# Kernel optimization log

Hardware: AMD Instinct MI355X
Metric: run time of the kernel (lower is better)

## Reference

```python
import jax, jax.numpy as jnp
import numpy as np

MARGIN = 0.2  # self.margin; temperature is unused in the original forward


def setup_inputs() -> dict:
    key = jax.random.key(0)
    k1, k2 = jax.random.split(key)
    B, D, NUM_CLASSES = 512, 256, 10
    features = jax.random.normal(k1, (B, D), dtype=jnp.float32)
    labels = jax.random.randint(k2, (B,), 0, NUM_CLASSES, dtype=jnp.int32)
    return {"features": features, "labels": labels}


def reference(features, labels):
    B = features.shape[0]
    sim = features @ features.T  # [B, B]

    eq = (labels[:, None] == labels[None, :])
    pos_mask = eq.astype(sim.dtype) * (1.0 - jnp.eye(B, dtype=sim.dtype))  # diag zeroed
    neg_mask = 1.0 - eq.astype(sim.dtype)

    # For anchor row i, pos j, neg k: relu(margin + sim[i,k] - sim[i,j])
    hinge = jax.nn.relu(MARGIN + sim[:, None, :] - sim[:, :, None])  # [B, Bpos, Bneg]
    loss_sum = jnp.einsum('ijk,ij,ik->', hinge, pos_mask, neg_mask)

    pos_cnt = pos_mask.sum(axis=1)  # per-row positive counts
    neg_cnt = neg_mask.sum(axis=1)
    valid = (pos_cnt > 0) & (neg_cnt > 0)
    num_valid = valid.sum().astype(sim.dtype)

    # Original bug faithfully reproduced: denominator uses the LAST row's
    # pos/neg counts (pos_sim/neg_sim leak out of the python loop).
    denom = num_valid * pos_cnt[-1] * neg_cnt[-1]
    return jnp.where(denom > 0, loss_sum / denom, jnp.zeros((), sim.dtype))
```

## Files before the change

kernel.cpp:

```cpp
#include <hip/hip_runtime.h>

#define B 512
#define D 256
#define NCLS 10
#define MARGIN 0.2f
#define THREADS 1024
#define NWAVES (THREADS / 64)
#define ROWS 2
#define NBLOCKS (B / ROWS)
#define DT 32
#define NDT (D / DT)
#define TILE_FLOATS (B * DT)

__global__ __launch_bounds__(THREADS) void fused_loss_kernel(
    const float* __restrict__ F, const int* __restrict__ labels,
    float* __restrict__ out)
{
    __shared__ float  buf[2][TILE_FLOATS];
    __shared__ float  fi[ROWS][D];
    __shared__ float  pos_vals[ROWS][B + 4];
    __shared__ float  neg_vals[ROWS][B];
    __shared__ int    lbl[B];
    __shared__ int    cnt[ROWS][2];
    __shared__ int    hist[NCLS];
    __shared__ float  wred[NWAVES];
    __shared__ int    vred[NWAVES];

    const int t    = threadIdx.x;
    const int lane = t & 63;
    const int w    = t >> 6;
    const int i0   = blockIdx.x * ROWS;
    const int q    = t & 3;
    const int g    = t >> 2;
    const int j0   = 2 * g;
    const int j1   = 2 * g + 1;
    const int s0   = (j0 & 7) ^ ((j0 >> 3) & 7);
    const int s1   = (j1 & 7) ^ ((j1 >> 3) & 7);

    auto stage = [&](float* dstbase, int tile) {
#pragma unroll
        for (int k = 0; k < 4; ++k) {
            const int p  = (w << 8) + (k << 6) + lane;
            const int jj = p >> 3;
            const int e4 = (p & 7) ^ (jj & 7) ^ ((jj >> 3) & 7);
            const float* src = F + jj * D + tile * DT + (e4 << 2);
            float* dst = dstbase + (w << 10) + (k << 8);
            __builtin_amdgcn_global_load_lds(
                (const __attribute__((address_space(1))) void*)src,
                (__attribute__((address_space(3))) void*)dst, 16, 0, 0);
        }
    };

    if (t < B)        lbl[t] = labels[t];
    if (t < NCLS)     hist[t] = 0;
    if (t < ROWS * 2) ((int*)cnt)[t] = 0;
    if (t < (ROWS * D) / 4)
        ((float4*)fi)[t] = ((const float4*)(F + (size_t)i0 * D))[t];
    stage(buf[0], 0);

    asm volatile("s_waitcnt lgkmcnt(0)" ::: "memory");
    __builtin_amdgcn_s_barrier();

    if (t < B) atomicAdd(&hist[lbl[t]], 1);

    float acc00 = 0.f, acc01 = 0.f, acc10 = 0.f, acc11 = 0.f;
    int cur = 0;
    for (int tile = 0; tile < NDT; ++tile) {
        if (tile + 1 < NDT) {
            stage(buf[cur ^ 1], tile + 1);
            asm volatile("s_waitcnt vmcnt(4)" ::: "memory");
        } else {
            asm volatile("s_waitcnt vmcnt(0)" ::: "memory");
        }
        __builtin_amdgcn_s_barrier();
        __builtin_amdgcn_sched_barrier(0);
        const float* bufc = buf[cur];
        const int dt = tile * DT;
#pragma unroll
        for (int k = 0; k < 2; ++k) {
            const int e4 = 2 * q + k;
            const float4 x0 = *(const float4*)&bufc[(j0 << 5) + ((e4 ^ s0) << 2)];
            const float4 x1 = *(const float4*)&bufc[(j1 << 5) + ((e4 ^ s1) << 2)];
            const float4 a0 = *(const float4*)&fi[0][dt + (e4 << 2)];
            const float4 a1 = *(const float4*)&fi[1][dt + (e4 << 2)];
            acc00 = fmaf(a0.x, x0.x, acc00); acc00 = fmaf(a0.y, x0.y, acc00);
            acc00 = fmaf(a0.z, x0.z, acc00); acc00 = fmaf(a0.w, x0.w, acc00);
            acc01 = fmaf(a1.x, x0.x, acc01); acc01 = fmaf(a1.y, x0.y, acc01);
            acc01 = fmaf(a1.z, x0.z, acc01); acc01 = fmaf(a1.w, x0.w, acc01);
            acc10 = fmaf(a0.x, x1.x, acc10); acc10 = fmaf(a0.y, x1.y, acc10);
            acc10 = fmaf(a0.z, x1.z, acc10); acc10 = fmaf(a0.w, x1.w, acc10);
            acc11 = fmaf(a1.x, x1.x, acc11); acc11 = fmaf(a1.y, x1.y, acc11);
            acc11 = fmaf(a1.z, x1.z, acc11); acc11 = fmaf(a1.w, x1.w, acc11);
        }
        __builtin_amdgcn_sched_barrier(0);
        __builtin_amdgcn_s_barrier();
        cur ^= 1;
    }

    float2* part = (float2*)buf[0];
    part[(q << 9) + j0] = make_float2(acc00, acc01);
    part[(q << 9) + j1] = make_float2(acc10, acc11);
    __syncthreads();
    const int j = t & (B - 1);
    const int h = t >> 9;
    const float2 p0 = part[(0 << 9) + j];
    const float2 p1 = part[(1 << 9) + j];
    const float2 p2 = part[(2 << 9) + j];
    const float2 p3 = part[(3 << 9) + j];
    const float sv = h ? (p0.y + p1.y + p2.y + p3.y)
                       : (p0.x + p1.x + p2.x + p3.x);

    {
        bool valid = false;
        if (t < B) { const int c = hist[lbl[t]]; valid = (c >= 2) && (c <= B - 1); }
        const unsigned long long mv = __ballot(valid);
        if (lane == 0) vred[w] = __popcll(mv);
    }

    const int r   = h;
    const int i_r = i0 + r;
    const int li  = lbl[i_r];
    {
        const bool active = (j != i_r);
        const bool ispos  = active && (lbl[j] == li);
        const bool isneg  = active && (lbl[j] != li);
        const unsigned long long mp = __ballot(ispos);
        const unsigned long long mn = __ballot(isneg);
        int basep = 0, basen = 0;
        if (lane == 0) {
            basep = atomicAdd(&cnt[r][0], __popcll(mp));
            basen = atomicAdd(&cnt[r][1], __popcll(mn));
        }
        basep = __shfl(basep, 0, 64);
        basen = __shfl(basen, 0, 64);
        const unsigned long long below = (1ull << lane) - 1ull;
        if (ispos) pos_vals[r][basep + __popcll(mp & below)] = sv;
        if (isneg) neg_vals[r][basen + __popcll(mn & below)] = sv;
    }
    __syncthreads();
    const int P = cnt[r][0], N = cnt[r][1];
    if (j < 4) pos_vals[r][P + j] = 1e30f;
    __syncthreads();

    const float nv_t = (j < N) ? neg_vals[r][j] : -1e30f;
    float local = 0.f;
    for (int pi = 0; pi < P; pi += 4) {
        const float4 pv = *(const float4*)&pos_vals[r][pi];
        float v;
        v = nv_t - (pv.x - MARGIN); local += (v > 0.f) ? v : 0.f;
        v = nv_t - (pv.y - MARGIN); local += (v > 0.f) ? v : 0.f;
        v = nv_t - (pv.z - MARGIN); local += (v > 0.f) ? v : 0.f;
        v = nv_t - (pv.w - MARGIN); local += (v > 0.f) ? v : 0.f;
    }

#pragma unroll
    for (int off = 32; off > 0; off >>= 1)
        local += __shfl_down(local, off, 64);
    if (lane == 0) wred[w] = local;
    __syncthreads();
    if (t == 0) {
        float s = 0.f;
        int   nv = 0;
#pragma unroll
        for (int k = 0; k < NWAVES; ++k) { s += wred[k]; nv += vred[k]; }
        const int   clast = hist[lbl[B - 1]];
        const float denom = (float)nv * (float)(clast - 1) * (float)(B - clast);
        atomicAdd(out, (denom > 0.f) ? s / denom : 0.f);
    }
}

extern "C" void kernel_launch(void* const* d_in, const int* in_sizes, int n_in,
                              void* d_out, int out_size, void* d_ws, size_t ws_size,
                              hipStream_t stream) {
    const float* F      = (const float*)d_in[0];
    const int*   labels = (const int*)d_in[1];
    float* out = (float*)d_out;
    (void)d_ws; (void)ws_size;

    fused_loss_kernel<<<NBLOCKS, THREADS, 0, stream>>>(F, labels, out);
}
```

Before: 67.87 us.

## Load anchor rows via scalar loads and remap threads to wave-uniform k-slices

Removes the LDS copy of the two anchor feature rows. Each wave now reads its anchor-row slice directly into scalar registers with s_load_dwordx4, which relies on the thread-to-work mapping being redone so the quarter of the k dimension (rq) is uniform across a wave. Per-tile LDS traffic drops to just the column tiles, and the anchor values come from SGPRs at the cost of scalar-cache loads every tile and an explicit lgkmcnt wait. The change also shifts the column-tile bank-access pattern, which could affect conflicts.

```diff
diff --git a/kernel.cpp b/kernel.cpp
--- a/kernel.cpp
+++ b/kernel.cpp
@@ -12,12 +12,13 @@
 #define NDT (D / DT)
 #define TILE_FLOATS (B * DT)
 
+typedef float f32x4 __attribute__((ext_vector_type(4)));
+
 __global__ __launch_bounds__(THREADS) void fused_loss_kernel(
     const float* __restrict__ F, const int* __restrict__ labels,
     float* __restrict__ out)
 {
     __shared__ float  buf[2][TILE_FLOATS];
-    __shared__ float  fi[ROWS][D];
     __shared__ float  pos_vals[ROWS][B + 4];
     __shared__ float  neg_vals[ROWS][B];
     __shared__ int    lbl[B];
@@ -30,8 +31,8 @@
     const int lane = t & 63;
     const int w    = t >> 6;
     const int i0   = blockIdx.x * ROWS;
-    const int q    = t & 3;
-    const int g    = t >> 2;
+    const int rq   = __builtin_amdgcn_readfirstlane(w & 3);
+    const int g    = ((w >> 2) << 6) + lane;
     const int j0   = 2 * g;
     const int j1   = 2 * g + 1;
     const int s0   = (j0 & 7) ^ ((j0 >> 3) & 7);
@@ -54,14 +55,15 @@
     if (t < B)        lbl[t] = labels[t];
     if (t < NCLS)     hist[t] = 0;
     if (t < ROWS * 2) ((int*)cnt)[t] = 0;
-    if (t < (ROWS * D) / 4)
-        ((float4*)fi)[t] = ((const float4*)(F + (size_t)i0 * D))[t];
     stage(buf[0], 0);
 
     asm volatile("s_waitcnt lgkmcnt(0)" ::: "memory");
     __builtin_amdgcn_s_barrier();
 
     if (t < B) atomicAdd(&hist[lbl[t]], 1);
+
+    const uint64_t sbase =
+        (uint64_t)(const void*)(F + (size_t)i0 * D + 8 * rq);
 
     float acc00 = 0.f, acc01 = 0.f, acc10 = 0.f, acc11 = 0.f;
     int cur = 0;
@@ -74,32 +76,51 @@
         }
         __builtin_amdgcn_s_barrier();
         __builtin_amdgcn_sched_barrier(0);
+
+        const uint64_t sb = sbase + (uint64_t)(tile * DT * 4);
+        f32x4 a00, a01, a10, a11;
+        asm volatile("s_load_dwordx4 %0, %1, 0x0"   : "=s"(a00) : "s"(sb));
+        asm volatile("s_load_dwordx4 %0, %1, 0x10"  : "=s"(a01) : "s"(sb));
+        asm volatile("s_load_dwordx4 %0, %1, 0x400" : "=s"(a10) : "s"(sb));
+        asm volatile("s_load_dwordx4 %0, %1, 0x410" : "=s"(a11) : "s"(sb));
+
         const float* bufc = buf[cur];
-        const int dt = tile * DT;
-#pragma unroll
-        for (int k = 0; k < 2; ++k) {
-            const int e4 = 2 * q + k;
-            const float4 x0 = *(const float4*)&bufc[(j0 << 5) + ((e4 ^ s0) << 2)];
-            const float4 x1 = *(const float4*)&bufc[(j1 << 5) + ((e4 ^ s1) << 2)];
-            const float4 a0 = *(const float4*)&fi[0][dt + (e4 << 2)];
-            const float4 a1 = *(const float4*)&fi[1][dt + (e4 << 2)];
-            acc00 = fmaf(a0.x, x0.x, acc00); acc00 = fmaf(a0.y, x0.y, acc00);
-            acc00 = fmaf(a0.z, x0.z, acc00); acc00 = fmaf(a0.w, x0.w, acc00);
-            acc01 = fmaf(a1.x, x0.x, acc01); acc01 = fmaf(a1.y, x0.y, acc01);
-            acc01 = fmaf(a1.z, x0.z, acc01); acc01 = fmaf(a1.w, x0.w, acc01);
-            acc10 = fmaf(a0.x, x1.x, acc10); acc10 = fmaf(a0.y, x1.y, acc10);
-            acc10 = fmaf(a0.z, x1.z, acc10); acc10 = fmaf(a0.w, x1.w, acc10);
-            acc11 = fmaf(a1.x, x1.x, acc11); acc11 = fmaf(a1.y, x1.y, acc11);
-            acc11 = fmaf(a1.z, x1.z, acc11); acc11 = fmaf(a1.w, x1.w, acc11);
-        }
+        const int e40 = 2 * rq;
+        const int e41 = 2 * rq + 1;
+        const float4 x00 = *(const float4*)&bufc[(j0 << 5) + ((e40 ^ s0) << 2)];
+        const float4 x01 = *(const float4*)&bufc[(j0 << 5) + ((e41 ^ s0) << 2)];
+        const float4 x10 = *(const float4*)&bufc[(j1 << 5) + ((e40 ^ s1) << 2)];
+        const float4 x11 = *(const float4*)&bufc[(j1 << 5) + ((e41 ^ s1) << 2)];
+
+        asm volatile("s_waitcnt lgkmcnt(0)" ::: "memory");
+        __builtin_amdgcn_sched_barrier(0);
+
+        acc00 = fmaf(a00.x, x00.x, acc00); acc00 = fmaf(a00.y, x00.y, acc00);
+        acc00 = fmaf(a00.z, x00.z, acc00); acc00 = fmaf(a00.w, x00.w, acc00);
+        acc01 = fmaf(a10.x, x00.x, acc01); acc01 = fmaf(a10.y, x00.y, acc01);
+        acc01 = fmaf(a10.z, x00.z, acc01); acc01 = fmaf(a10.w, x00.w, acc01);
+        acc10 = fmaf(a00.x, x10.x, acc10); acc10 = fmaf(a00.y, x10.y, acc10);
+        acc10 = fmaf(a00.z, x10.z, acc10); acc10 = fmaf(a00.w, x10.w, acc10);
+        acc11 = fmaf(a10.x, x10.x, acc11); acc11 = fmaf(a10.y, x10.y, acc11);
+        acc11 = fmaf(a10.z, x10.z, acc11); acc11 = fmaf(a10.w, x10.w, acc11);
+
+        acc00 = fmaf(a01.x, x01.x, acc00); acc00 = fmaf(a01.y, x01.y, acc00);
+        acc00 = fmaf(a01.z, x01.z, acc00); acc00 = fmaf(a01.w, x01.w, acc00);
+        acc01 = fmaf(a11.x, x01.x, acc01); acc01 = fmaf(a11.y, x01.y, acc01);
+        acc01 = fmaf(a11.z, x01.z, acc01); acc01 = fmaf(a11.w, x01.w, acc01);
+        acc10 = fmaf(a01.x, x11.x, acc10); acc10 = fmaf(a01.y, x11.y, acc10);
+        acc10 = fmaf(a01.z, x11.z, acc10); acc10 = fmaf(a01.w, x11.w, acc10);
+        acc11 = fmaf(a11.x, x11.x, acc11); acc11 = fmaf(a11.y, x11.y, acc11);
+        acc11 = fmaf(a11.z, x11.z, acc11); acc11 = fmaf(a11.w, x11.w, acc11);
+
         __builtin_amdgcn_sched_barrier(0);
         __builtin_amdgcn_s_barrier();
         cur ^= 1;
     }
 
     float2* part = (float2*)buf[0];
-    part[(q << 9) + j0] = make_float2(acc00, acc01);
-    part[(q << 9) + j1] = make_float2(acc10, acc11);
+    part[(rq << 9) + j0] = make_float2(acc00, acc01);
+    part[(rq << 9) + j1] = make_float2(acc10, acc11);
     __syncthreads();
     const int j = t & (B - 1);
     const int h = t >> 9;
```

Result: no change. 69.02 us (+1.7%).
